# Performance work log

Hardware: AMD Instinct MI355X
Metric: run time of the kernel (lower is better)

## Reference

```python
import jax, jax.numpy as jnp
import numpy as np
from jax import lax
import math

B, C, H, W = 8, 512, 24, 24
L = H * W
D_STATE = 16
D_INNER = 2 * C
DT_RANK = C // 16
K = 4
SCALE = 1.0 / math.sqrt(C)


def layer_norm(x, g, b, eps=1e-5):
    m = x.mean(-1, keepdims=True)
    v = ((x - m) ** 2).mean(-1, keepdims=True)
    return (x - m) * lax.rsqrt(v + eps) * g + b


def selective_scan(u, delta, A, Bm, Cm, Ds):
    # u, delta: (B,K,d,L); Bm, Cm: (B,K,N,L); A: (K,d,N); Ds: (K,d)
    us = jnp.moveaxis(u, -1, 0)      # (L,B,K,d)
    dts = jnp.moveaxis(delta, -1, 0)
    Bs = jnp.moveaxis(Bm, -1, 0)     # (L,B,K,N)
    Cs = jnp.moveaxis(Cm, -1, 0)

    def step(h, inp):
        u_t, dt_t, B_t, C_t = inp
        dA = jnp.exp(dt_t[..., None] * A)                      # (B,K,d,N)
        dBu = (dt_t * u_t)[..., None] * B_t[:, :, None, :]     # (B,K,d,N)
        h = dA * h + dBu
        y = jnp.einsum('bkdn,bkn->bkd', h, C_t)
        return h, y

    h0 = jnp.zeros(u.shape[:3] + (A.shape[-1],), u.dtype)
    _, ys = lax.scan(step, h0, (us, dts, Bs, Cs))
    y = jnp.moveaxis(ys, 0, -1)                                # (B,K,d,L)
    return y + Ds[None, :, :, None] * u


def ss2d(x, in_proj_w, dwconv_w, dwconv_b, x_proj_w, dt_proj_w, dt_proj_b,
         A_logs, Ds, out_norm_g, out_norm_b, out_proj_w):
    # x: (B,H,W,C) channel-last
    xz = x @ in_proj_w.T                                       # (B,H,W,2*d_inner)
    xi, z = jnp.split(xz, 2, axis=-1)
    xc = xi.transpose(0, 3, 1, 2)                              # (B,d_inner,H,W)
    xc = lax.conv_general_dilated(xc, dwconv_w, (1, 1), 'SAME',
                                  feature_group_count=D_INNER,
                                  dimension_numbers=('NCHW', 'OIHW', 'NCHW'))
    xc = jax.nn.silu(xc + dwconv_b[None, :, None, None])
    x_hw = xc.reshape(B, D_INNER, L)
    x_wh = xc.transpose(0, 1, 3, 2).reshape(B, D_INNER, L)
    xs = jnp.stack([x_hw, x_wh, x_hw[..., ::-1], x_wh[..., ::-1]], axis=1)  # (B,4,d,L)
    x_dbl = jnp.einsum('bkdl,kcd->bkcl', xs, x_proj_w)
    dt, Bm, Cm = jnp.split(x_dbl, [DT_RANK, DT_RANK + D_STATE], axis=2)
    delta = jax.nn.softplus(jnp.einsum('bkrl,kdr->bkdl', dt, dt_proj_w)
                            + dt_proj_b[None, :, :, None])
    A = -jnp.exp(A_logs)
    ys = selective_scan(xs, delta, A, Bm, Cm, Ds)              # (B,4,d,L)
    y_wh = ys[:, 1].reshape(B, D_INNER, W, H).transpose(0, 1, 3, 2).reshape(B, D_INNER, L)
    y_whr = ys[:, 3, :, ::-1].reshape(B, D_INNER, W, H).transpose(0, 1, 3, 2).reshape(B, D_INNER, L)
    y = ys[:, 0] + ys[:, 2, :, ::-1] + y_wh + y_whr
    y = y.reshape(B, D_INNER, H, W).transpose(0, 2, 3, 1)      # (B,H,W,d_inner)
    y = layer_norm(y, out_norm_g, out_norm_b)
    y = y * jax.nn.silu(z)
    return y @ out_proj_w.T                                    # (B,H,W,C)


def setup_inputs():
    key = jax.random.key(0)
    ks = jax.random.split(key, 10)
    n = lambda k, sh, s=0.02: jax.random.normal(k, sh, dtype=jnp.float32) * s
    return {
        'x5': jax.random.normal(ks[0], (B, C, H, W), dtype=jnp.float32),
        'conv_w': n(ks[1], (C, C)),
        'conv_b': jnp.zeros((C,), jnp.float32),
        'ln1_g': jnp.ones((C,), jnp.float32),
        'ln1_b': jnp.zeros((C,), jnp.float32),
        'in_proj_w': n(ks[2], (2 * D_INNER, C)),
        'dwconv_w': n(ks[3], (D_INNER, 1, 3, 3), 0.1),
        'dwconv_b': jnp.zeros((D_INNER,), jnp.float32),
        'x_proj_w': n(ks[4], (K, DT_RANK + 2 * D_STATE, D_INNER)),
        'dt_proj_w': n(ks[5], (K, D_INNER, DT_RANK), 0.1),
        'dt_proj_b': n(ks[6], (K, D_INNER), 0.1),
        'A_logs': jnp.tile(jnp.log(jnp.arange(1, D_STATE + 1, dtype=jnp.float32))[None, None, :],
                           (K, D_INNER, 1)),
        'Ds': jnp.ones((K, D_INNER), jnp.float32),
        'out_norm_g': jnp.ones((D_INNER,), jnp.float32),
        'out_norm_b': jnp.zeros((D_INNER,), jnp.float32),
        'out_proj_w': n(ks[7], (C, D_INNER)),
    }


def reference(x5, conv_w, conv_b, ln1_g, ln1_b, in_proj_w, dwconv_w, dwconv_b,
              x_proj_w, dt_proj_w, dt_proj_b, A_logs, Ds, out_norm_g, out_norm_b,
              out_proj_w):
    # 1x1 conv + residual
    x5 = jnp.einsum('bchw,oc->bohw', x5, conv_w) + conv_b[None, :, None, None] + x5
    x0 = x5.transpose(0, 2, 3, 1)                              # (B,H,W,C)
    # VSSBlock: x + SS2D(LN(x)); called twice on same input with same weights -> identical
    x00 = x0 + ss2d(layer_norm(x0, ln1_g, ln1_b), in_proj_w, dwconv_w, dwconv_b,
                    x_proj_w, dt_proj_w, dt_proj_b, A_logs, Ds,
                    out_norm_g, out_norm_b, out_proj_w)
    xq = x00.transpose(0, 3, 1, 2).reshape(B, C, L)            # (B,C,L)
    xq_flat = xq.transpose(0, 2, 1).reshape(B * L, C)          # (B*L, C)
    xk_flat = xq.transpose(1, 0, 2).reshape(C, B * L)          # (C, B*L)
    xw = (xq_flat @ xk_flat) * SCALE                           # (B*L, B*L)
    xw = xw.reshape(B * L, B, L).max(-1).mean(-1).reshape(B, L)
    xw = jax.nn.softmax(xw, axis=-1)
    norm0 = x5 / jnp.maximum(jnp.linalg.norm(x5, axis=1, keepdims=True), 1e-12)
    xw = xw[:, None, :]                                        # (B,1,L)
    xw_max = xw.max(-1, keepdims=True)
    mask = (xw == xw_max).astype(x5.dtype).reshape(B, 1, H, W)  # winner-take-all
    seeds = (norm0 * mask).sum((2, 3))                         # (B,C)
    # correlation (eval branch: relu), seeds act as 1x1 conv weights
    cor = jax.nn.relu(jnp.einsum('bchw,oc->bohw', norm0, seeds)).mean(1).reshape(B, L)
    mn = cor.min(1, keepdims=True)
    mx = cor.max(1, keepdims=True)
    cormap = ((cor - mn) / (mx - mn + 1e-12)).reshape(B, 1, H, W)
    x51 = x5 * cormap
    proto1 = x51.mean((0, 2, 3), keepdims=True)                # (1,C,1,1)
    return (x5, proto1, x5 * proto1 + x51, mask)
```

## Files before the change

### kernel.cpp

```cpp
#include <hip/hip_runtime.h>
#include <math.h>

#define NB 8
#define NC 512
#define NH 24
#define NW 24
#define NL 576
#define ND 1024
#define NBL 4608
#define NCH 8
#define CL 72

static constexpr float SCALE_ = 0.044194173824159216f;

typedef __attribute__((ext_vector_type(8))) short bf16x8;
typedef __attribute__((ext_vector_type(4))) float f32x4;

__device__ __forceinline__ unsigned enc_f(float f){
    unsigned u = __float_as_uint(f);
    return (u & 0x80000000u) ? ~u : (u | 0x80000000u);
}
__device__ __forceinline__ float dec_f(unsigned e){
    return (e & 0x80000000u) ? __uint_as_float(e ^ 0x80000000u) : __uint_as_float(~e);
}

__device__ __forceinline__ int scan_idx(int t, int k){
    int t2 = (k >= 2) ? (NL - 1 - t) : t;
    return (k & 1) ? ((t2 % NH) * NW + t2 / NH) : t2;
}

__device__ __forceinline__ float softplus_f(float x){
    return fmaxf(x, 0.f) + __logf(1.f + __expf(-fabsf(x)));
}
__device__ __forceinline__ float silu_f(float x){
    return x / (1.f + __expf(-x));
}

__device__ __forceinline__ void split_bf(float v, unsigned short &h, unsigned short &l){
    unsigned u = __float_as_uint(v);
    unsigned hr = (u + 0x7fffu + ((u>>16)&1u)) >> 16;
    h = (unsigned short)hr;
    float hf = __uint_as_float(hr << 16);
    unsigned u2 = __float_as_uint(v - hf);
    l = (unsigned short)((u2 + 0x7fffu + ((u2>>16)&1u)) >> 16);
}

__global__ void k_transpose_in(const float* __restrict__ x5, float* __restrict__ x5t,
                               unsigned short* __restrict__ x5tB){
    __shared__ float t[32][33];
    const int b = blockIdx.z;
    const int c0 = blockIdx.x*32, l0 = blockIdx.y*32;
    const int tx = threadIdx.x & 31, ty = threadIdx.x >> 5;
    #pragma unroll
    for (int i=ty; i<32; i+=8)
        t[i][tx] = x5[((size_t)b*NC + c0 + i)*NL + l0 + tx];
    __syncthreads();
    #pragma unroll
    for (int i=ty; i<32; i+=8){
        float v = t[tx][i];
        x5t[((size_t)b*NL + l0 + i)*NC + c0 + tx] = v;
        unsigned short hh, ll; split_bf(v, hh, ll);
        size_t rb = ((size_t)b*NL + l0 + i)*1536 + c0 + tx;
        x5tB[rb] = hh; x5tB[rb+512] = ll; x5tB[rb+1024] = hh;
    }
}

template<int FORM>
__global__ void k_split(const float* __restrict__ in, unsigned short* __restrict__ oA,
                        unsigned short* __restrict__ oB, int K, int total4){
    int t = blockIdx.x*256 + threadIdx.x;
    if (t >= total4) return;
    int kq = K >> 2;
    int r = t / kq; int k4 = (t - r*kq) << 2;
    float4 v = *(const float4*)(in + (size_t)r*K + k4);
    float vv[4] = {v.x, v.y, v.z, v.w};
    unsigned short h[4], lo[4];
    #pragma unroll
    for (int i=0;i<4;i++) split_bf(vv[i], h[i], lo[i]);
    unsigned hp0 = h[0] | ((unsigned)h[1]<<16), hp1 = h[2] | ((unsigned)h[3]<<16);
    unsigned lp0 = lo[0] | ((unsigned)lo[1]<<16), lp1 = lo[2] | ((unsigned)lo[3]<<16);
    size_t base = (size_t)r*3*K + k4;
    if (FORM == 0 || FORM == 2){
        unsigned* p0 = (unsigned*)(oA + base);
        unsigned* p1 = (unsigned*)(oA + base + K);
        unsigned* p2 = (unsigned*)(oA + base + 2*K);
        p0[0]=hp0; p0[1]=hp1;  p1[0]=hp0; p1[1]=hp1;  p2[0]=lp0; p2[1]=lp1;
    }
    if (FORM == 1 || FORM == 2){
        unsigned short* o = (FORM==2) ? oB : oA;
        unsigned* p0 = (unsigned*)(o + base);
        unsigned* p1 = (unsigned*)(o + base + K);
        unsigned* p2 = (unsigned*)(o + base + 2*K);
        p0[0]=hp0; p0[1]=hp1;  p1[0]=lp0; p1[1]=lp1;  p2[0]=hp0; p2[1]=hp1;
    }
}

template<int MODE>
__launch_bounds__(256)
__global__ void mfma_nt(const unsigned short* __restrict__ A, const unsigned short* __restrict__ Bm,
                        const float* __restrict__ R0, const float* __restrict__ R1,
                        float* __restrict__ out0, float* __restrict__ out1,
                        unsigned* __restrict__ mbuf, int K3)
{
    int bi, bj;
    if (MODE == 4){
        int rem = blockIdx.x, len = 36; bi = 0;
        while (rem >= len){ rem -= len; len--; bi++; }
        bj = bi + rem;
    } else { bi = blockIdx.x; bj = blockIdx.y; }
    const int m0 = bi*128, n0 = bj*128;
    __shared__ __align__(16) unsigned short As[128*32];
    __shared__ __align__(16) unsigned short Bs[128*32];
    const int tid = threadIdx.x;
    const int w = tid >> 6, l = tid & 63;
    const int mw = (w>>1)*64, nw = (w&1)*64;
    const int fr = l & 15, fq = l >> 4;

    f32x4 acc[4][4];
    #pragma unroll
    for (int i=0;i<4;i++)
        #pragma unroll
        for (int j=0;j<4;j++)
            #pragma unroll
            for (int c=0;c<4;c++) acc[i][j][c] = 0.f;

    const int c0 = tid, c1 = tid + 256;
    const int r0 = c0 >> 2, o0 = (c0 & 3) * 8;
    const int r1 = c1 >> 2, o1 = (c1 & 3) * 8;
    const unsigned short* pA0 = A  + (size_t)(m0 + r0)*K3 + o0;
    const unsigned short* pA1 = A  + (size_t)(m0 + r1)*K3 + o1;
    const unsigned short* pB0 = Bm + (size_t)(n0 + r0)*K3 + o0;
    const unsigned short* pB1 = Bm + (size_t)(n0 + r1)*K3 + o1;

    float4 a0 = *(const float4*)(pA0);
    float4 a1 = *(const float4*)(pA1);
    float4 b0 = *(const float4*)(pB0);
    float4 b1 = *(const float4*)(pB1);

    for (int k0 = 0; k0 < K3; k0 += 32){
        __syncthreads();
        *(float4*)&As[c0*8] = a0;
        *(float4*)&As[c1*8] = a1;
        *(float4*)&Bs[c0*8] = b0;
        *(float4*)&Bs[c1*8] = b1;
        __syncthreads();
        if (k0 + 32 < K3){
            a0 = *(const float4*)(pA0 + k0 + 32);
            a1 = *(const float4*)(pA1 + k0 + 32);
            b0 = *(const float4*)(pB0 + k0 + 32);
            b1 = *(const float4*)(pB1 + k0 + 32);
        }
        bf16x8 af[4], bf[4];
        #pragma unroll
        for (int i=0;i<4;i++){
            af[i] = *(const bf16x8*)&As[(mw + i*16 + fr)*32 + fq*8];
            bf[i] = *(const bf16x8*)&Bs[(nw + i*16 + fr)*32 + fq*8];
        }
        #pragma unroll
        for (int i=0;i<4;i++)
            #pragma unroll
            for (int j=0;j<4;j++)
                acc[i][j] = __builtin_amdgcn_mfma_f32_16x16x32_bf16(af[i], bf[j], acc[i][j], 0, 0, 0);
    }

    if (MODE == 4){
        const int b2c = (n0 + nw) / NL;
        #pragma unroll
        for (int mi=0; mi<4; mi++){
            #pragma unroll
            for (int i=0;i<4;i++){
                float v = fmaxf(fmaxf(acc[mi][0][i], acc[mi][1][i]),
                                fmaxf(acc[mi][2][i], acc[mi][3][i]));
                v = fmaxf(v, __shfl_xor(v, 1));
                v = fmaxf(v, __shfl_xor(v, 2));
                v = fmaxf(v, __shfl_xor(v, 4));
                v = fmaxf(v, __shfl_xor(v, 8));
                if (fr == 0)
                    atomicMax(&mbuf[(size_t)(m0 + mw + mi*16 + fq*4 + i)*NB + b2c], enc_f(v));
            }
        }
        const int b2r = (m0 + mw) / NL;
        #pragma unroll
        for (int ni=0; ni<4; ni++){
            float cm = -3.4e38f;
            #pragma unroll
            for (int mi=0; mi<4; mi++)
                #pragma unroll
                for (int i=0;i<4;i++) cm = fmaxf(cm, acc[mi][ni][i]);
            cm = fmaxf(cm, __shfl_xor(cm, 16));
            cm = fmaxf(cm, __shfl_xor(cm, 32));
            if (fq == 0)
                atomicMax(&mbuf[(size_t)(n0 + nw + ni*16 + fr)*NB + b2r], enc_f(cm));
        }
        return;
    }

    #pragma unroll
    for (int mi=0; mi<4; mi++){
        const int m = m0 + mw + mi*16 + fq*4;
        #pragma unroll
        for (int ni=0; ni<4; ni++){
            const int n = n0 + nw + ni*16 + fr;
            f32x4 a = acc[mi][ni];
            if (MODE == 0){
                float4 cb = *(const float4*)(R0 + m);
                float4 rs = *(const float4*)(R1 + (size_t)n*NC + m);
                float4 ov = make_float4(a[0]+cb.x+rs.x, a[1]+cb.y+rs.y, a[2]+cb.z+rs.z, a[3]+cb.w+rs.w);
                *(float4*)(out0 + (size_t)n*NC + m) = ov;
            } else if (MODE == 1){
                float4 ov = make_float4(a[0], a[1], a[2], a[3]);
                if (m < ND) *(float4*)(out0 + (size_t)n*ND + m) = ov;
                else        *(float4*)(out1 + (size_t)n*ND + (m - ND)) = ov;
            } else {
                float4 rs = *(const float4*)(R1 + (size_t)n*NC + m);
                float4 ov = make_float4(a[0]+rs.x, a[1]+rs.y, a[2]+rs.z, a[3]+rs.w);
                *(float4*)(out0 + (size_t)n*NC + m) = ov;
            }
        }
    }
}

template<int MODE>
__launch_bounds__(256)
__global__ void gemm_nt(const float* __restrict__ A0, const float* __restrict__ B0,
                        const float* __restrict__ R,
                        float* __restrict__ out0, float* __restrict__ out1,
                        unsigned* __restrict__ mbuf, int K)
{
    __shared__ __align__(16) float As[16][68];
    __shared__ __align__(16) float Bs[16][68];
    const int tid = threadIdx.x;
    const int m0 = blockIdx.x * 64;
    const int n0 = blockIdx.y * 64;
    const float* A = A0;
    const float* B = B0;
    int kdir = 0;
    if (MODE == 2) {
        const int bk = blockIdx.z;
        kdir = bk & 3; const int bb = bk >> 2;
        A = A0 + (size_t)kdir * 64 * 1024;
        B = B0 + (size_t)bb * NL * 1024;
    }
    const int lrow = tid >> 2;
    const int lk4  = (tid & 3) << 2;
    int brow = n0 + lrow;
    if (MODE == 2) brow = scan_idx(brow, kdir);
    const float* aptr = A + (size_t)(m0 + lrow) * K + lk4;
    const float* bptr = B + (size_t)brow * K + lk4;

    float acc[4][4];
    #pragma unroll
    for (int i=0;i<4;i++){
        #pragma unroll
        for (int j=0;j<4;j++) acc[i][j]=0.f;
    }
    const int tx = tid & 15, ty = tid >> 4;

    for (int k0 = 0; k0 < K; k0 += 16) {
        float4 av = *(const float4*)(aptr + k0);
        float4 bv = *(const float4*)(bptr + k0);
        __syncthreads();
        As[lk4+0][lrow]=av.x; As[lk4+1][lrow]=av.y; As[lk4+2][lrow]=av.z; As[lk4+3][lrow]=av.w;
        Bs[lk4+0][lrow]=bv.x; Bs[lk4+1][lrow]=bv.y; Bs[lk4+2][lrow]=bv.z; Bs[lk4+3][lrow]=bv.w;
        __syncthreads();
        #pragma unroll
        for (int kk=0;kk<16;kk++){
            float4 a = *(const float4*)&As[kk][ty<<2];
            float4 b = *(const float4*)&Bs[kk][tx<<2];
            acc[0][0] = fmaf(a.x,b.x,acc[0][0]); acc[0][1] = fmaf(a.x,b.y,acc[0][1]);
            acc[0][2] = fmaf(a.x,b.z,acc[0][2]); acc[0][3] = fmaf(a.x,b.w,acc[0][3]);
            acc[1][0] = fmaf(a.y,b.x,acc[1][0]); acc[1][1] = fmaf(a.y,b.y,acc[1][1]);
            acc[1][2] = fmaf(a.y,b.z,acc[1][2]); acc[1][3] = fmaf(a.y,b.w,acc[1][3]);
            acc[2][0] = fmaf(a.z,b.x,acc[2][0]); acc[2][1] = fmaf(a.z,b.y,acc[2][1]);
            acc[2][2] = fmaf(a.z,b.z,acc[2][2]); acc[2][3] = fmaf(a.z,b.w,acc[2][3]);
            acc[3][0] = fmaf(a.w,b.x,acc[3][0]); acc[3][1] = fmaf(a.w,b.y,acc[3][1]);
            acc[3][2] = fmaf(a.w,b.z,acc[3][2]); acc[3][3] = fmaf(a.w,b.w,acc[3][3]);
        }
    }

    #pragma unroll
    for (int j=0;j<4;j++){
        const int n  = n0 + (tx<<2) + j;
        const int mm = m0 + (ty<<2);
        float4 v = make_float4(acc[0][j], acc[1][j], acc[2][j], acc[3][j]);
        if (MODE == 2){
            *(float4*)(out0 + ((size_t)blockIdx.z*NL + n)*64 + mm) = v;
        }
    }
}

__global__ void k_ln512b(const float* __restrict__ x, const float* __restrict__ g,
                         const float* __restrict__ bb, unsigned short* __restrict__ outB){
    int n = blockIdx.x; int tid = threadIdx.x;
    const float* row = x + (size_t)n*NC;
    float v0 = row[tid], v1 = row[tid+256];
    __shared__ float s1[256], s2[256];
    s1[tid] = v0+v1; s2[tid] = v0*v0 + v1*v1;
    __syncthreads();
    for (int s=128;s>0;s>>=1){ if (tid<s){ s1[tid]+=s1[tid+s]; s2[tid]+=s2[tid+s]; } __syncthreads(); }
    float mean = s1[0]*(1.f/NC);
    float var  = fmaxf(s2[0]*(1.f/NC) - mean*mean, 0.f);
    float rs   = rsqrtf(var + 1e-5f);
    float r0 = (v0-mean)*rs*g[tid]     + bb[tid];
    float r1 = (v1-mean)*rs*g[tid+256] + bb[tid+256];
    unsigned short h0,l0,h1,l1; split_bf(r0,h0,l0); split_bf(r1,h1,l1);
    size_t base = (size_t)n*1536;
    outB[base+tid]     =h0; outB[base+512+tid]     =l0; outB[base+1024+tid]     =h0;
    outB[base+tid+256] =h1; outB[base+512+tid+256] =l1; outB[base+1024+tid+256] =h1;
}

__global__ void k_dwconv(const float* __restrict__ xi, const float* __restrict__ w,
                         const float* __restrict__ bias, float* __restrict__ xcl){
    int d = blockIdx.x*256 + threadIdx.x;
    int h = blockIdx.y; int b = blockIdx.z;
    float W[9];
    #pragma unroll
    for (int i=0;i<9;i++) W[i] = w[d*9+i];
    float bs = bias[d];
    const size_t rb = ((size_t)b*NL)*ND + d;
    const bool hm = h > 0, hp = h < NH-1;
    float p0=0.f,p1=0.f,p2=0.f;
    float c0 = hm ? xi[rb + (size_t)((h-1)*NW)*ND] : 0.f;
    float c1 = xi[rb + (size_t)(h*NW)*ND];
    float c2 = hp ? xi[rb + (size_t)((h+1)*NW)*ND] : 0.f;
    for (int wc=0; wc<NW; wc++){
        float n0,n1,n2;
        if (wc < NW-1){
            n0 = hm ? xi[rb + (size_t)((h-1)*NW+wc+1)*ND] : 0.f;
            n1 = xi[rb + (size_t)(h*NW+wc+1)*ND];
            n2 = hp ? xi[rb + (size_t)((h+1)*NW+wc+1)*ND] : 0.f;
        } else { n0=0.f;n1=0.f;n2=0.f; }
        float acc = bs;
        acc = fmaf(W[0],p0, fmaf(W[1],c0, fmaf(W[2],n0, acc)));
        acc = fmaf(W[3],p1, fmaf(W[4],c1, fmaf(W[5],n1, acc)));
        acc = fmaf(W[6],p2, fmaf(W[7],c2, fmaf(W[8],n2, acc)));
        xcl[rb + (size_t)(h*NW+wc)*ND] = silu_f(acc);
        p0=c0;p1=c1;p2=c2; c0=n0;c1=n1;c2=n2;
    }
}

#define DA_POWERS \
    float e2=e1*e1; float e3=e2*e1; float e4=e2*e2; \
    float e6=e4*e2; float e7=e4*e3; float e8=e4*e4; float e12=e8*e4; \
    float dA[16]; \
    dA[0]=e1; dA[1]=e2; dA[2]=e3; dA[3]=e4; dA[4]=e4*e1; dA[5]=e6; dA[6]=e7; dA[7]=e8; \
    dA[8]=e8*e1; dA[9]=e8*e2; dA[10]=e8*e3; dA[11]=e12; dA[12]=e12*e1; dA[13]=e12*e2; \
    dA[14]=e12*e3; dA[15]=e8*e8;

#define DOT4(rq, dtb, out) { \
    float4 q0=rq[0],q1=rq[1],q2=rq[2],q3=rq[3],q4=rq[4],q5=rq[5],q6=rq[6],q7=rq[7]; \
    float s0=0.f,s1=0.f,s2=0.f,s3=0.f; \
    s0=fmaf(q0.x,wdt[0],s0);  s1=fmaf(q0.y,wdt[1],s1);  s2=fmaf(q0.z,wdt[2],s2);  s3=fmaf(q0.w,wdt[3],s3); \
    s0=fmaf(q1.x,wdt[4],s0);  s1=fmaf(q1.y,wdt[5],s1);  s2=fmaf(q1.z,wdt[6],s2);  s3=fmaf(q1.w,wdt[7],s3); \
    s0=fmaf(q2.x,wdt[8],s0);  s1=fmaf(q2.y,wdt[9],s1);  s2=fmaf(q2.z,wdt[10],s2); s3=fmaf(q2.w,wdt[11],s3); \
    s0=fmaf(q3.x,wdt[12],s0); s1=fmaf(q3.y,wdt[13],s1); s2=fmaf(q3.z,wdt[14],s2); s3=fmaf(q3.w,wdt[15],s3); \
    s0=fmaf(q4.x,wdt[16],s0); s1=fmaf(q4.y,wdt[17],s1); s2=fmaf(q4.z,wdt[18],s2); s3=fmaf(q4.w,wdt[19],s3); \
    s0=fmaf(q5.x,wdt[20],s0); s1=fmaf(q5.y,wdt[21],s1); s2=fmaf(q5.z,wdt[22],s2); s3=fmaf(q5.w,wdt[23],s3); \
    s0=fmaf(q6.x,wdt[24],s0); s1=fmaf(q6.y,wdt[25],s1); s2=fmaf(q6.z,wdt[26],s2); s3=fmaf(q6.w,wdt[27],s3); \
    s0=fmaf(q7.x,wdt[28],s0); s1=fmaf(q7.y,wdt[29],s1); s2=fmaf(q7.z,wdt[30],s2); s3=fmaf(q7.w,wdt[31],s3); \
    out = (s0+s1)+(s2+s3)+dtb; }

__launch_bounds__(128)
__global__ void k_scan_p1(const float* __restrict__ xcl, const float* __restrict__ xdbl,
                          const float* __restrict__ dtw, const float* __restrict__ dtb,
                          const float* __restrict__ alogs,
                          float* __restrict__ hfin, float* __restrict__ prodA){
    const int d = blockIdx.x*128 + threadIdx.x;
    const int chunk = blockIdx.y;
    const int bk = blockIdx.z;
    const int k = bk & 3, b = bk >> 2;
    const int kd = k*ND + d;
    float wdt[32];
    {
        const float4* p = (const float4*)(dtw + (size_t)kd*32);
        #pragma unroll
        for (int i=0;i<8;i++){ float4 v=p[i]; wdt[4*i]=v.x; wdt[4*i+1]=v.y; wdt[4*i+2]=v.z; wdt[4*i+3]=v.w; }
    }
    float An[16]; bool ladder = true;
    {
        const float4* p = (const float4*)(alogs + (size_t)kd*16);
        #pragma unroll
        for (int i=0;i<4;i++){
            float4 v=p[i];
            An[4*i]=-__expf(v.x); An[4*i+1]=-__expf(v.y); An[4*i+2]=-__expf(v.z); An[4*i+3]=-__expf(v.w);
        }
        #pragma unroll
        for (int n=0;n<16;n++) ladder = ladder && (fabsf(An[n] + (float)(n+1)) < 1e-3f*(n+1));
    }
    const float dtbias = dtb[kd];
    __shared__ __align__(16) float rows[CL*64];
    {
        const float4* src = (const float4*)(xdbl + ((size_t)bk*NL + chunk*CL)*64);
        for (int i = threadIdx.x; i < CL*16; i += 128) ((float4*)rows)[i] = src[i];
    }
    __syncthreads();
    float h[16], pA[16];
    #pragma unroll
    for (int n=0;n<16;n++){ h[n]=0.f; pA[n]=1.f; }
    if (ladder){
        float u = xcl[((size_t)b*NL + scan_idx(chunk*CL, k))*ND + d];
        for (int t=0;t<CL;t++){
            const float4* rq = (const float4*)(rows + t*64);
            float dr; DOT4(rq, dtbias, dr);
            float u_cur = u;
            if (t+1 < CL) u = xcl[((size_t)b*NL + scan_idx(chunk*CL+t+1, k))*ND + d];
            float sp = softplus_f(dr);
            float du = sp * u_cur;
            float e1 = __expf(-sp);
            DA_POWERS
            float4 B0=rq[8],B1=rq[9],B2=rq[10],B3=rq[11];
            const float Bv[16] = {B0.x,B0.y,B0.z,B0.w,B1.x,B1.y,B1.z,B1.w,
                                  B2.x,B2.y,B2.z,B2.w,B3.x,B3.y,B3.z,B3.w};
            #pragma unroll
            for (int n=0;n<16;n++){
                pA[n] *= dA[n];
                h[n] = fmaf(dA[n], h[n], du*Bv[n]);
            }
        }
    } else {
        for (int t=0;t<CL;t++){
            const float4* rq = (const float4*)(rows + t*64);
            float dr; DOT4(rq, dtbias, dr);
            float sp = softplus_f(dr);
            int idx = scan_idx(chunk*CL + t, k);
            float u  = xcl[((size_t)b*NL + idx)*ND + d];
            float du = sp * u;
            const float* row = rows + t*64;
            #pragma unroll
            for (int n=0;n<16;n++){
                float dA = __expf(sp * An[n]);
                pA[n] *= dA;
                h[n] = fmaf(dA, h[n], du*row[32+n]);
            }
        }
    }
    size_t base = (size_t)(bk*NCH + chunk)*16*1024 + d;
    #pragma unroll
    for (int n=0;n<16;n++){ hfin[base + n*1024] = h[n]; prodA[base + n*1024] = pA[n]; }
}

__global__ void k_scan_mid(float* __restrict__ hfin, const float* __restrict__ prodA){
    int id = blockIdx.x*256 + threadIdx.x;
    int d = id & 1023, nn = (id >> 10) & 15, bk = id >> 14;
    float h = 0.f;
    for (int j=0;j<NCH;j++){
        size_t idx = (size_t)((bk*NCH + j)*16 + nn)*1024 + d;
        float hf = hfin[idx], pa = prodA[idx];
        hfin[idx] = h;
        h = fmaf(pa, h, hf);
    }
}

__launch_bounds__(128)
__global__ void k_scan_p2(const float* __restrict__ xcl, const float* __restrict__ xdbl,
                          const float* __restrict__ dtw, const float* __restrict__ dtb,
                          const float* __restrict__ alogs,
                          const float* __restrict__ hfin, float* __restrict__ yacc){
    const int d = blockIdx.x*128 + threadIdx.x;
    const int chunk = blockIdx.y;
    const int bk = blockIdx.z;
    const int k = bk & 3, b = bk >> 2;
    const int kd = k*ND + d;
    float wdt[32];
    {
        const float4* p = (const float4*)(dtw + (size_t)kd*32);
        #pragma unroll
        for (int i=0;i<8;i++){ float4 v=p[i]; wdt[4*i]=v.x; wdt[4*i+1]=v.y; wdt[4*i+2]=v.z; wdt[4*i+3]=v.w; }
    }
    float An[16]; bool ladder = true;
    {
        const float4* p = (const float4*)(alogs + (size_t)kd*16);
        #pragma unroll
        for (int i=0;i<4;i++){
            float4 v=p[i];
            An[4*i]=-__expf(v.x); An[4*i+1]=-__expf(v.y); An[4*i+2]=-__expf(v.z); An[4*i+3]=-__expf(v.w);
        }
        #pragma unroll
        for (int n=0;n<16;n++) ladder = ladder && (fabsf(An[n] + (float)(n+1)) < 1e-3f*(n+1));
    }
    const float dtbias = dtb[kd];
    __shared__ __align__(16) float rows[CL*64];
    {
        const float4* src = (const float4*)(xdbl + ((size_t)bk*NL + chunk*CL)*64);
        for (int i = threadIdx.x; i < CL*16; i += 128) ((float4*)rows)[i] = src[i];
    }
    __syncthreads();
    float h[16];
    {
        size_t base = (size_t)(bk*NCH + chunk)*16*1024 + d;
        #pragma unroll
        for (int n=0;n<16;n++) h[n] = hfin[base + n*1024];
    }
    if (ladder){
        int idx = scan_idx(chunk*CL, k);
        float u = xcl[((size_t)b*NL + idx)*ND + d];
        for (int t=0;t<CL;t++){
            const float4* rq = (const float4*)(rows + t*64);
            float dr; DOT4(rq, dtbias, dr);
            float u_cur = u; int idx_cur = idx;
            if (t+1 < CL){
                idx = scan_idx(chunk*CL+t+1, k);
                u = xcl[((size_t)b*NL + idx)*ND + d];
            }
            float sp = softplus_f(dr);
            float du = sp * u_cur;
            float e1 = __expf(-sp);
            DA_POWERS
            float4 B0=rq[8],B1=rq[9],B2=rq[10],B3=rq[11];
            float4 C0=rq[12],C1=rq[13],C2=rq[14],C3=rq[15];
            const float Bv[16] = {B0.x,B0.y,B0.z,B0.w,B1.x,B1.y,B1.z,B1.w,
                                  B2.x,B2.y,B2.z,B2.w,B3.x,B3.y,B3.z,B3.w};
            const float Cv[16] = {C0.x,C0.y,C0.z,C0.w,C1.x,C1.y,C1.z,C1.w,
                                  C2.x,C2.y,C2.z,C2.w,C3.x,C3.y,C3.z,C3.w};
            float y0=0.f, y1=0.f;
            #pragma unroll
            for (int n=0;n<16;n++){
                h[n] = fmaf(dA[n], h[n], du*Bv[n]);
                if (n & 1) y1 = fmaf(h[n], Cv[n], y1); else y0 = fmaf(h[n], Cv[n], y0);
            }
            atomicAdd(&yacc[((size_t)b*NL + idx_cur)*ND + d], y0+y1);
        }
    } else {
        for (int t=0;t<CL;t++){
            const float4* rq = (const float4*)(rows + t*64);
            float dr; DOT4(rq, dtbias, dr);
            float sp = softplus_f(dr);
            int idx = scan_idx(chunk*CL + t, k);
            size_t base = ((size_t)b*NL + idx)*ND + d;
            float u  = xcl[base];
            float du = sp * u;
            const float* row = rows + t*64;
            float y = 0.f;
            #pragma unroll
            for (int n=0;n<16;n++){
                float dA = __expf(sp * An[n]);
                h[n] = fmaf(dA, h[n], du*row[32+n]);
                y = fmaf(h[n], row[48+n], y);
            }
            atomicAdd(&yacc[base], y);
        }
    }
}

__global__ void k_combine(const float* __restrict__ y, const float* __restrict__ xcl,
                          const float* __restrict__ Ds,
                          const float* __restrict__ g, const float* __restrict__ bb,
                          const float* __restrict__ z, unsigned short* __restrict__ zB){
    int n = blockIdx.x;
    size_t base = (size_t)n*ND;
    int tid = threadIdx.x;
    float v[4]; float sum=0.f, sq=0.f;
    #pragma unroll
    for (int j=0;j<4;j++){
        int d = tid + 256*j;
        float ds = Ds[d] + Ds[ND+d] + Ds[2*ND+d] + Ds[3*ND+d];
        float val = y[base+d] + ds*xcl[base+d];
        v[j]=val; sum+=val; sq+=val*val;
    }
    __shared__ float s1[256], s2[256];
    s1[tid]=sum; s2[tid]=sq; __syncthreads();
    for (int st=128;st>0;st>>=1){ if(tid<st){ s1[tid]+=s1[tid+st]; s2[tid]+=s2[tid+st]; } __syncthreads(); }
    float mean = s1[0]*(1.f/ND);
    float var  = fmaxf(s2[0]*(1.f/ND) - mean*mean, 0.f);
    float rs   = rsqrtf(var + 1e-5f);
    size_t zb = (size_t)n*3072;
    #pragma unroll
    for (int j=0;j<4;j++){
        int d = tid + 256*j;
        float ln = (v[j]-mean)*rs*g[d] + bb[d];
        float res = ln * silu_f(z[base+d]);
        unsigned short hh,ll; split_bf(res,hh,ll);
        zB[zb + d] = hh; zB[zb + 1024 + d] = ll; zB[zb + 2048 + d] = hh;
    }
}

__global__ void k_xwpre(const unsigned* __restrict__ M, float* __restrict__ xwp){
    int n = blockIdx.x*256 + threadIdx.x; if (n >= NBL) return;
    float sum = 0.f;
    #pragma unroll
    for (int b2=0;b2<NB;b2++) sum += dec_f(M[(size_t)n*NB + b2]);
    xwp[n] = sum * (SCALE_/8.f);
}

__global__ void k_mask(const float* __restrict__ xwp, float* __restrict__ maskf){
    int b = blockIdx.x; int tid = threadIdx.x;
    float m = -1e30f;
    for (int i=tid;i<NL;i+=64) m = fmaxf(m, xwp[b*NL+i]);
    __shared__ float s1[64];
    s1[tid]=m; __syncthreads();
    for (int st=32;st>0;st>>=1){ if(tid<st) s1[tid]=fmaxf(s1[tid],s1[tid+st]); __syncthreads(); }
    float bm = s1[0];
    for (int i=tid;i<NL;i+=64) maskf[b*NL+i] = (xwp[b*NL+i]==bm) ? 1.f : 0.f;
}

__global__ void k_norm0(const float* __restrict__ x5r, float* __restrict__ norm0){
    int n = blockIdx.x; int tid = threadIdx.x;
    float v0 = x5r[(size_t)n*NC+tid], v1 = x5r[(size_t)n*NC+tid+256];
    __shared__ float s1[256];
    s1[tid] = v0*v0 + v1*v1; __syncthreads();
    for (int st=128;st>0;st>>=1){ if(tid<st) s1[tid]+=s1[tid+st]; __syncthreads(); }
    float inv = 1.f / fmaxf(sqrtf(s1[0]), 1e-12f);
    norm0[(size_t)n*NC+tid]     = v0*inv;
    norm0[(size_t)n*NC+tid+256] = v1*inv;
}

__global__ void k_seeds(const float* __restrict__ norm0, const float* __restrict__ maskf,
                        float* __restrict__ seeds){
    int b = blockIdx.x; int c = threadIdx.x;
    float acc = 0.f;
    for (int l=0;l<NL;l++){
        float mk = maskf[b*NL+l];
        if (mk != 0.f) acc += norm0[((size_t)b*NL+l)*NC + c]*mk;
    }
    seeds[b*NC + c] = acc;
}

__global__ void k_cor(const float* __restrict__ norm0, const float* __restrict__ seeds,
                      float* __restrict__ cor){
    int n = blockIdx.x; int tid = threadIdx.x;
    int o = tid >> 6, lane = tid & 63;
    float acc = 0.f;
    #pragma unroll
    for (int i=0;i<8;i++){
        int c = lane + 64*i;
        acc += norm0[(size_t)n*NC + c] * seeds[o*NC + c];
    }
    #pragma unroll
    for (int s=32;s>0;s>>=1) acc += __shfl_xor(acc, s);
    __shared__ float sr[8];
    if (lane == 0) sr[o] = fmaxf(acc, 0.f);
    __syncthreads();
    if (tid == 0){
        float r = 0.f;
        #pragma unroll
        for (int o2=0;o2<8;o2++) r += sr[o2];
        cor[n] = r * (1.f/8.f);
    }
}

__global__ void k_cormap(const float* __restrict__ cor, float* __restrict__ cmap){
    int b = blockIdx.x, tid = threadIdx.x;
    float mn = 1e30f, mx = -1e30f;
    for (int i=tid;i<NL;i+=64){ float v=cor[b*NL+i]; mn=fminf(mn,v); mx=fmaxf(mx,v); }
    __shared__ float sn[64], sx[64];
    sn[tid]=mn; sx[tid]=mx; __syncthreads();
    for (int st=32;st>0;st>>=1){ if(tid<st){ sn[tid]=fminf(sn[tid],sn[tid+st]); sx[tid]=fmaxf(sx[tid],sx[tid+st]); } __syncthreads(); }
    float MN=sn[0], MX=sx[0];
    float inv = 1.f/(MX-MN+1e-12f);
    for (int i=tid;i<NL;i+=64) cmap[b*NL+i] = (cor[b*NL+i]-MN)*inv;
}

__global__ void k_proto(const float* __restrict__ x5r, const float* __restrict__ cmap,
                        float* __restrict__ pacc){
    int c = threadIdx.x;
    int chunk = blockIdx.x;
    float acc = 0.f;
    for (int i=0;i<64;i++){
        int n = chunk*64 + i;
        acc += x5r[(size_t)n*NC + c] * cmap[n];
    }
    atomicAdd(&pacc[c], acc);
}

__global__ void k_final(const float* __restrict__ x5r, const float* __restrict__ cmap,
                        const float* __restrict__ pacc, const float* __restrict__ maskf,
                        float* __restrict__ out){
    int id = blockIdx.x*256 + threadIdx.x;
    int l = id % NL; int bc = id / NL; int c = bc & 511; int b = bc >> 9;
    float v  = x5r[((size_t)b*NL + l)*NC + c];
    float p  = pacc[c] * (1.f/(float)NBL);
    float cm = cmap[b*NL + l];
    out[id] = v;
    out[2359296 + 512 + id] = v*(p + cm);
    if (id < 512)  out[2359296 + id] = pacc[id] * (1.f/(float)NBL);
    if (id < NBL)  out[2359296 + 512 + 2359296 + id] = maskf[id];
}

extern "C" void kernel_launch(void* const* d_in, const int* in_sizes, int n_in,
                              void* d_out, int out_size, void* d_ws, size_t ws_size,
                              hipStream_t stream) {
    const float* x5        = (const float*)d_in[0];
    const float* conv_w    = (const float*)d_in[1];
    const float* conv_b    = (const float*)d_in[2];
    const float* ln1_g     = (const float*)d_in[3];
    const float* ln1_b     = (const float*)d_in[4];
    const float* in_proj_w = (const float*)d_in[5];
    const float* dwconv_w  = (const float*)d_in[6];
    const float* dwconv_b  = (const float*)d_in[7];
    const float* x_proj_w  = (const float*)d_in[8];
    const float* dt_proj_w = (const float*)d_in[9];
    const float* dt_proj_b = (const float*)d_in[10];
    const float* A_logs    = (const float*)d_in[11];
    const float* Ds        = (const float*)d_in[12];
    const float* out_norm_g= (const float*)d_in[13];
    const float* out_norm_b= (const float*)d_in[14];
    const float* out_proj_w= (const float*)d_in[15];

    float* ws = (float*)d_ws;
    const size_t O_X5R  = 0;
    const size_t O_XLN  = 2359296;
    const size_t O_XI   = 4718592;
    const size_t O_Z    = 9437184;
    const size_t O_XCL  = 14155776;
    const size_t O_XDBL = 18874368;
    const size_t O_HF   = 20054016;
    const size_t O_PA   = 24248320;
    const size_t O_MBUF = 28442624;
    const size_t O_XWP  = 28479488;
    const size_t O_MASK = 28484096;
    const size_t O_COR  = 28488704;
    const size_t O_CMAP = 28493312;
    const size_t O_SEED = 28497920;
    const size_t O_PACC = 28502016;

    float* x5r  = ws + O_X5R;
    float* xqf  = ws + O_XLN;
    float* xi   = ws + O_XI;
    float* yacc = ws + O_XI;
    unsigned short* wAo = (unsigned short*)(ws + O_XI);
    float* z    = ws + O_Z;
    float* xcl  = ws + O_XCL;
    unsigned short* wAi = (unsigned short*)(ws + O_XCL);
    float* nrm0 = ws + O_XCL;
    float* xdbl = ws + O_XDBL;
    float* x5t  = ws + O_HF;
    float* hfin = ws + O_HF;
    unsigned short* xlnB = (unsigned short*)(ws + O_HF);
    unsigned short* zB   = (unsigned short*)(ws + O_HF);
    unsigned short* xqfA = (unsigned short*)(ws + O_HF);
    float* prodA = ws + O_PA;
    unsigned short* x5tB = (unsigned short*)(ws + O_PA);
    unsigned short* wAc  = (unsigned short*)(ws + O_PA) + 7077888;
    unsigned short* xqfB = (unsigned short*)(ws + O_PA);
    unsigned* mbuf = (unsigned*)(ws + O_MBUF);
    float* xwp  = ws + O_XWP;
    float* maskf= ws + O_MASK;
    float* cor  = ws + O_COR;
    float* cmap = ws + O_CMAP;
    float* seeds= ws + O_SEED;
    float* pacc = ws + O_PACC;

    (void)hipMemsetAsync(mbuf, 0, 36864*sizeof(unsigned), stream);
    (void)hipMemsetAsync(pacc, 0, 512*sizeof(float), stream);

    k_transpose_in<<<dim3(16,18,8), 256, 0, stream>>>(x5, x5t, x5tB);
    k_split<0><<<256, 256, 0, stream>>>(conv_w, wAc, nullptr, 512, 65536);
    mfma_nt<0><<<dim3(4,36), 256, 0, stream>>>(wAc, x5tB, conv_b, x5t, x5r, nullptr, nullptr, 1536);
    k_ln512b<<<NBL, 256, 0, stream>>>(x5r, ln1_g, ln1_b, xlnB);
    k_split<0><<<1024, 256, 0, stream>>>(in_proj_w, wAi, nullptr, 512, 262144);
    mfma_nt<1><<<dim3(16,36), 256, 0, stream>>>(wAi, xlnB, nullptr, nullptr, xi, z, nullptr, 1536);
    k_dwconv<<<dim3(4,NH,NB), 256, 0, stream>>>(xi, dwconv_w, dwconv_b, xcl);
    (void)hipMemsetAsync(yacc, 0, (size_t)4718592*sizeof(float), stream);
    gemm_nt<2><<<dim3(1,9,32), 256, 0, stream>>>(x_proj_w, xcl, nullptr, xdbl, nullptr, nullptr, 1024);
    k_scan_p1<<<dim3(8,NCH,32), 128, 0, stream>>>(xcl, xdbl, dt_proj_w, dt_proj_b, A_logs, hfin, prodA);
    k_scan_mid<<<2048, 256, 0, stream>>>(hfin, prodA);
    k_scan_p2<<<dim3(8,NCH,32), 128, 0, stream>>>(xcl, xdbl, dt_proj_w, dt_proj_b, A_logs, hfin, yacc);
    k_combine<<<NBL, 256, 0, stream>>>(yacc, xcl, Ds, out_norm_g, out_norm_b, z, zB);
    k_split<0><<<512, 256, 0, stream>>>(out_proj_w, wAo, nullptr, 1024, 131072);
    mfma_nt<3><<<dim3(4,36), 256, 0, stream>>>(wAo, zB, nullptr, x5r, xqf, nullptr, nullptr, 3072);
    k_split<2><<<2304, 256, 0, stream>>>(xqf, xqfA, xqfB, 512, 589824);
    mfma_nt<4><<<666, 256, 0, stream>>>(xqfA, xqfB, nullptr, nullptr, nullptr, nullptr, mbuf, 1536);
    k_xwpre<<<18, 256, 0, stream>>>(mbuf, xwp);
    k_mask<<<NB, 64, 0, stream>>>(xwp, maskf);
    k_norm0<<<NBL, 256, 0, stream>>>(x5r, nrm0);
    k_seeds<<<NB, 512, 0, stream>>>(nrm0, maskf, seeds);
    k_cor<<<NBL, 512, 0, stream>>>(nrm0, seeds, cor);
    k_cormap<<<NB, 64, 0, stream>>>(cor, cmap);
    k_proto<<<72, 512, 0, stream>>>(x5r, cmap, pacc);
    k_final<<<9216, 256, 0, stream>>>(x5r, cmap, pacc, maskf, (float*)d_out);
}
```

Baseline: 652.0 us.

## Pack scan math into float2 vectors, fuse xw reduction into mask, sparse seeds

The scan kernels' ladder path now uses two-wide float vectors for the dt dot product, the dA powers, the state update and the output reduction, aiming to emit packed FP32 instructions on MI355X. The separate xw pre-reduction and mask kernels are merged into one kernel that also records the winning indices, saving one launch and one intermediate buffer. The seeds kernel then loops only over the recorded hits instead of all 576 positions. Floating-point summation order changes slightly, and hit order depends on shared atomics.

```diff
diff --git a/kernel.cpp b/kernel.cpp
--- a/kernel.cpp
+++ b/kernel.cpp
@@ -11,10 +11,9 @@
 #define NCH 8
 #define CL 72
 
-static constexpr float SCALE_ = 0.044194173824159216f;
-
 typedef __attribute__((ext_vector_type(8))) short bf16x8;
 typedef __attribute__((ext_vector_type(4))) float f32x4;
+typedef __attribute__((ext_vector_type(2))) float f32x2;
 
 __device__ __forceinline__ unsigned enc_f(float f){
     unsigned u = __float_as_uint(f);
@@ -339,26 +338,22 @@
     }
 }
 
-#define DA_POWERS \
+#define DA_POWERS2 \
     float e2=e1*e1; float e3=e2*e1; float e4=e2*e2; \
     float e6=e4*e2; float e7=e4*e3; float e8=e4*e4; float e12=e8*e4; \
-    float dA[16]; \
-    dA[0]=e1; dA[1]=e2; dA[2]=e3; dA[3]=e4; dA[4]=e4*e1; dA[5]=e6; dA[6]=e7; dA[7]=e8; \
-    dA[8]=e8*e1; dA[9]=e8*e2; dA[10]=e8*e3; dA[11]=e12; dA[12]=e12*e1; dA[13]=e12*e2; \
-    dA[14]=e12*e3; dA[15]=e8*e8;
-
-#define DOT4(rq, dtb, out) { \
-    float4 q0=rq[0],q1=rq[1],q2=rq[2],q3=rq[3],q4=rq[4],q5=rq[5],q6=rq[6],q7=rq[7]; \
-    float s0=0.f,s1=0.f,s2=0.f,s3=0.f; \
-    s0=fmaf(q0.x,wdt[0],s0);  s1=fmaf(q0.y,wdt[1],s1);  s2=fmaf(q0.z,wdt[2],s2);  s3=fmaf(q0.w,wdt[3],s3); \
-    s0=fmaf(q1.x,wdt[4],s0);  s1=fmaf(q1.y,wdt[5],s1);  s2=fmaf(q1.z,wdt[6],s2);  s3=fmaf(q1.w,wdt[7],s3); \
-    s0=fmaf(q2.x,wdt[8],s0);  s1=fmaf(q2.y,wdt[9],s1);  s2=fmaf(q2.z,wdt[10],s2); s3=fmaf(q2.w,wdt[11],s3); \
-    s0=fmaf(q3.x,wdt[12],s0); s1=fmaf(q3.y,wdt[13],s1); s2=fmaf(q3.z,wdt[14],s2); s3=fmaf(q3.w,wdt[15],s3); \
-    s0=fmaf(q4.x,wdt[16],s0); s1=fmaf(q4.y,wdt[17],s1); s2=fmaf(q4.z,wdt[18],s2); s3=fmaf(q4.w,wdt[19],s3); \
-    s0=fmaf(q5.x,wdt[20],s0); s1=fmaf(q5.y,wdt[21],s1); s2=fmaf(q5.z,wdt[22],s2); s3=fmaf(q5.w,wdt[23],s3); \
-    s0=fmaf(q6.x,wdt[24],s0); s1=fmaf(q6.y,wdt[25],s1); s2=fmaf(q6.z,wdt[26],s2); s3=fmaf(q6.w,wdt[27],s3); \
-    s0=fmaf(q7.x,wdt[28],s0); s1=fmaf(q7.y,wdt[29],s1); s2=fmaf(q7.z,wdt[30],s2); s3=fmaf(q7.w,wdt[31],s3); \
-    out = (s0+s1)+(s2+s3)+dtb; }
+    f32x2 dA2[8]; \
+    dA2[0]=(f32x2){e1,e2};       dA2[1]=(f32x2){e3,e4}; \
+    dA2[2]=(f32x2){e4*e1,e6};    dA2[3]=(f32x2){e7,e8}; \
+    dA2[4]=(f32x2){e8*e1,e8*e2}; dA2[5]=(f32x2){e8*e3,e12}; \
+    dA2[6]=(f32x2){e12*e1,e12*e2}; dA2[7]=(f32x2){e12*e3,e8*e8};
+
+#define DOT4P(rq2, dtb, out) { \
+    f32x2 sA={0.f,0.f},sB={0.f,0.f},sC={0.f,0.f},sD={0.f,0.f}; \
+    sA += rq2[0]*wdt2[0];  sB += rq2[1]*wdt2[1];  sC += rq2[2]*wdt2[2];  sD += rq2[3]*wdt2[3]; \
+    sA += rq2[4]*wdt2[4];  sB += rq2[5]*wdt2[5];  sC += rq2[6]*wdt2[6];  sD += rq2[7]*wdt2[7]; \
+    sA += rq2[8]*wdt2[8];  sB += rq2[9]*wdt2[9];  sC += rq2[10]*wdt2[10]; sD += rq2[11]*wdt2[11]; \
+    sA += rq2[12]*wdt2[12]; sB += rq2[13]*wdt2[13]; sC += rq2[14]*wdt2[14]; sD += rq2[15]*wdt2[15]; \
+    out = ((sA.x+sA.y)+(sB.x+sB.y)) + ((sC.x+sC.y)+(sD.x+sD.y)) + dtb; }
 
 __launch_bounds__(128)
 __global__ void k_scan_p1(const float* __restrict__ xcl, const float* __restrict__ xdbl,
@@ -370,11 +365,15 @@
     const int bk = blockIdx.z;
     const int k = bk & 3, b = bk >> 2;
     const int kd = k*ND + d;
-    float wdt[32];
+    f32x2 wdt2[16];
     {
         const float4* p = (const float4*)(dtw + (size_t)kd*32);
         #pragma unroll
-        for (int i=0;i<8;i++){ float4 v=p[i]; wdt[4*i]=v.x; wdt[4*i+1]=v.y; wdt[4*i+2]=v.z; wdt[4*i+3]=v.w; }
+        for (int i=0;i<8;i++){
+            float4 v=p[i];
+            wdt2[2*i]   = (f32x2){v.x, v.y};
+            wdt2[2*i+1] = (f32x2){v.z, v.w};
+        }
     }
     float An[16]; bool ladder = true;
     {
@@ -394,33 +393,40 @@
         for (int i = threadIdx.x; i < CL*16; i += 128) ((float4*)rows)[i] = src[i];
     }
     __syncthreads();
-    float h[16], pA[16];
-    #pragma unroll
-    for (int n=0;n<16;n++){ h[n]=0.f; pA[n]=1.f; }
     if (ladder){
+        f32x2 h2[8], pA2[8];
+        #pragma unroll
+        for (int n=0;n<8;n++){ h2[n]=(f32x2){0.f,0.f}; pA2[n]=(f32x2){1.f,1.f}; }
         float u = xcl[((size_t)b*NL + scan_idx(chunk*CL, k))*ND + d];
         for (int t=0;t<CL;t++){
-            const float4* rq = (const float4*)(rows + t*64);
-            float dr; DOT4(rq, dtbias, dr);
+            const f32x2* rq2 = (const f32x2*)(rows + t*64);
+            float dr; DOT4P(rq2, dtbias, dr);
             float u_cur = u;
             if (t+1 < CL) u = xcl[((size_t)b*NL + scan_idx(chunk*CL+t+1, k))*ND + d];
             float sp = softplus_f(dr);
             float du = sp * u_cur;
             float e1 = __expf(-sp);
-            DA_POWERS
-            float4 B0=rq[8],B1=rq[9],B2=rq[10],B3=rq[11];
-            const float Bv[16] = {B0.x,B0.y,B0.z,B0.w,B1.x,B1.y,B1.z,B1.w,
-                                  B2.x,B2.y,B2.z,B2.w,B3.x,B3.y,B3.z,B3.w};
-            #pragma unroll
-            for (int n=0;n<16;n++){
-                pA[n] *= dA[n];
-                h[n] = fmaf(dA[n], h[n], du*Bv[n]);
+            DA_POWERS2
+            f32x2 du2 = (f32x2){du, du};
+            #pragma unroll
+            for (int n=0;n<8;n++){
+                pA2[n] *= dA2[n];
+                h2[n] = dA2[n]*h2[n] + du2*rq2[16+n];
             }
         }
+        size_t base = (size_t)(bk*NCH + chunk)*16*1024 + d;
+        #pragma unroll
+        for (int n=0;n<8;n++){
+            hfin[base + (2*n)*1024]   = h2[n].x;  hfin[base + (2*n+1)*1024] = h2[n].y;
+            prodA[base + (2*n)*1024]  = pA2[n].x; prodA[base + (2*n+1)*1024]= pA2[n].y;
+        }
     } else {
+        float h[16], pA[16];
+        #pragma unroll
+        for (int n=0;n<16;n++){ h[n]=0.f; pA[n]=1.f; }
         for (int t=0;t<CL;t++){
-            const float4* rq = (const float4*)(rows + t*64);
-            float dr; DOT4(rq, dtbias, dr);
+            const f32x2* rq2 = (const f32x2*)(rows + t*64);
+            float dr; DOT4P(rq2, dtbias, dr);
             float sp = softplus_f(dr);
             int idx = scan_idx(chunk*CL + t, k);
             float u  = xcl[((size_t)b*NL + idx)*ND + d];
@@ -433,10 +439,10 @@
                 h[n] = fmaf(dA, h[n], du*row[32+n]);
             }
         }
-    }
-    size_t base = (size_t)(bk*NCH + chunk)*16*1024 + d;
-    #pragma unroll
-    for (int n=0;n<16;n++){ hfin[base + n*1024] = h[n]; prodA[base + n*1024] = pA[n]; }
+        size_t base = (size_t)(bk*NCH + chunk)*16*1024 + d;
+        #pragma unroll
+        for (int n=0;n<16;n++){ hfin[base + n*1024] = h[n]; prodA[base + n*1024] = pA[n]; }
+    }
 }
 
 __global__ void k_scan_mid(float* __restrict__ hfin, const float* __restrict__ prodA){
@@ -461,11 +467,15 @@
     const int bk = blockIdx.z;
     const int k = bk & 3, b = bk >> 2;
     const int kd = k*ND + d;
-    float wdt[32];
+    f32x2 wdt2[16];
     {
         const float4* p = (const float4*)(dtw + (size_t)kd*32);
         #pragma unroll
-        for (int i=0;i<8;i++){ float4 v=p[i]; wdt[4*i]=v.x; wdt[4*i+1]=v.y; wdt[4*i+2]=v.z; wdt[4*i+3]=v.w; }
+        for (int i=0;i<8;i++){
+            float4 v=p[i];
+            wdt2[2*i]   = (f32x2){v.x, v.y};
+            wdt2[2*i+1] = (f32x2){v.z, v.w};
+        }
     }
     float An[16]; bool ladder = true;
     {
@@ -485,18 +495,19 @@
         for (int i = threadIdx.x; i < CL*16; i += 128) ((float4*)rows)[i] = src[i];
     }
     __syncthreads();
-    float h[16];
-    {
-        size_t base = (size_t)(bk*NCH + chunk)*16*1024 + d;
-        #pragma unroll
-        for (int n=0;n<16;n++) h[n] = hfin[base + n*1024];
-    }
     if (ladder){
+        f32x2 h2[8];
+        {
+            size_t base = (size_t)(bk*NCH + chunk)*16*1024 + d;
+            #pragma unroll
+            for (int n=0;n<8;n++)
+                h2[n] = (f32x2){hfin[base + (2*n)*1024], hfin[base + (2*n+1)*1024]};
+        }
         int idx = scan_idx(chunk*CL, k);
         float u = xcl[((size_t)b*NL + idx)*ND + d];
         for (int t=0;t<CL;t++){
-            const float4* rq = (const float4*)(rows + t*64);
-            float dr; DOT4(rq, dtbias, dr);
+            const f32x2* rq2 = (const f32x2*)(rows + t*64);
+            float dr; DOT4P(rq2, dtbias, dr);
             float u_cur = u; int idx_cur = idx;
             if (t+1 < CL){
                 idx = scan_idx(chunk*CL+t+1, k);
@@ -505,25 +516,26 @@
             float sp = softplus_f(dr);
             float du = sp * u_cur;
             float e1 = __expf(-sp);
-            DA_POWERS
-            float4 B0=rq[8],B1=rq[9],B2=rq[10],B3=rq[11];
-            float4 C0=rq[12],C1=rq[13],C2=rq[14],C3=rq[15];
-            const float Bv[16] = {B0.x,B0.y,B0.z,B0.w,B1.x,B1.y,B1.z,B1.w,
-                                  B2.x,B2.y,B2.z,B2.w,B3.x,B3.y,B3.z,B3.w};
-            const float Cv[16] = {C0.x,C0.y,C0.z,C0.w,C1.x,C1.y,C1.z,C1.w,
-                                  C2.x,C2.y,C2.z,C2.w,C3.x,C3.y,C3.z,C3.w};
-            float y0=0.f, y1=0.f;
-            #pragma unroll
-            for (int n=0;n<16;n++){
-                h[n] = fmaf(dA[n], h[n], du*Bv[n]);
-                if (n & 1) y1 = fmaf(h[n], Cv[n], y1); else y0 = fmaf(h[n], Cv[n], y0);
+            DA_POWERS2
+            f32x2 du2 = (f32x2){du, du};
+            f32x2 y2 = (f32x2){0.f, 0.f};
+            #pragma unroll
+            for (int n=0;n<8;n++){
+                h2[n] = dA2[n]*h2[n] + du2*rq2[16+n];
+                y2 += h2[n]*rq2[24+n];
             }
-            atomicAdd(&yacc[((size_t)b*NL + idx_cur)*ND + d], y0+y1);
+            atomicAdd(&yacc[((size_t)b*NL + idx_cur)*ND + d], y2.x + y2.y);
         }
     } else {
+        float h[16];
+        {
+            size_t base = (size_t)(bk*NCH + chunk)*16*1024 + d;
+            #pragma unroll
+            for (int n=0;n<16;n++) h[n] = hfin[base + n*1024];
+        }
         for (int t=0;t<CL;t++){
-            const float4* rq = (const float4*)(rows + t*64);
-            float dr; DOT4(rq, dtbias, dr);
+            const f32x2* rq2 = (const f32x2*)(rows + t*64);
+            float dr; DOT4P(rq2, dtbias, dr);
             float sp = softplus_f(dr);
             int idx = scan_idx(chunk*CL + t, k);
             size_t base = ((size_t)b*NL + idx)*ND + d;
@@ -574,23 +586,36 @@
     }
 }
 
-__global__ void k_xwpre(const unsigned* __restrict__ M, float* __restrict__ xwp){
-    int n = blockIdx.x*256 + threadIdx.x; if (n >= NBL) return;
-    float sum = 0.f;
-    #pragma unroll
-    for (int b2=0;b2<NB;b2++) sum += dec_f(M[(size_t)n*NB + b2]);
-    xwp[n] = sum * (SCALE_/8.f);
-}
-
-__global__ void k_mask(const float* __restrict__ xwp, float* __restrict__ maskf){
+__global__ void k_mask2(const unsigned* __restrict__ M, float* __restrict__ maskf,
+                        int* __restrict__ hitcnt, int* __restrict__ hitidx){
     int b = blockIdx.x; int tid = threadIdx.x;
-    float m = -1e30f;
-    for (int i=tid;i<NL;i+=64) m = fmaxf(m, xwp[b*NL+i]);
-    __shared__ float s1[64];
-    s1[tid]=m; __syncthreads();
-    for (int st=32;st>0;st>>=1){ if(tid<st) s1[tid]=fmaxf(s1[tid],s1[tid+st]); __syncthreads(); }
-    float bm = s1[0];
-    for (int i=tid;i<NL;i+=64) maskf[b*NL+i] = (xwp[b*NL+i]==bm) ? 1.f : 0.f;
+    __shared__ int lcnt;
+    if (tid == 0) lcnt = 0;
+    __syncthreads();
+    float loc[9];
+    float m = -3.4e38f;
+    #pragma unroll
+    for (int j=0;j<9;j++){
+        int l = tid + j*64;
+        float s = 0.f;
+        #pragma unroll
+        for (int b2=0;b2<NB;b2++) s += dec_f(M[(size_t)(b*NL+l)*NB + b2]);
+        loc[j] = s; m = fmaxf(m, s);
+    }
+    #pragma unroll
+    for (int s=32;s>0;s>>=1) m = fmaxf(m, __shfl_xor(m, s));
+    #pragma unroll
+    for (int j=0;j<9;j++){
+        int l = tid + j*64;
+        bool hit = (loc[j] == m);
+        maskf[b*NL + l] = hit ? 1.f : 0.f;
+        if (hit){
+            int pos = atomicAdd(&lcnt, 1);
+            hitidx[b*NL + pos] = l;
+        }
+    }
+    __syncthreads();
+    if (tid == 0) hitcnt[b] = lcnt;
 }
 
 __global__ void k_norm0(const float* __restrict__ x5r, float* __restrict__ norm0){
@@ -604,13 +629,14 @@
     norm0[(size_t)n*NC+tid+256] = v1*inv;
 }
 
-__global__ void k_seeds(const float* __restrict__ norm0, const float* __restrict__ maskf,
-                        float* __restrict__ seeds){
+__global__ void k_seeds(const float* __restrict__ norm0, const int* __restrict__ hitcnt,
+                        const int* __restrict__ hitidx, float* __restrict__ seeds){
     int b = blockIdx.x; int c = threadIdx.x;
+    int cnt = hitcnt[b];
     float acc = 0.f;
-    for (int l=0;l<NL;l++){
-        float mk = maskf[b*NL+l];
-        if (mk != 0.f) acc += norm0[((size_t)b*NL+l)*NC + c]*mk;
+    for (int i=0;i<cnt;i++){
+        int l = hitidx[b*NL + i];
+        acc += norm0[((size_t)b*NL+l)*NC + c];
     }
     seeds[b*NC + c] = acc;
 }
@@ -706,12 +732,13 @@
     const size_t O_HF   = 20054016;
     const size_t O_PA   = 24248320;
     const size_t O_MBUF = 28442624;
-    const size_t O_XWP  = 28479488;
     const size_t O_MASK = 28484096;
     const size_t O_COR  = 28488704;
     const size_t O_CMAP = 28493312;
     const size_t O_SEED = 28497920;
     const size_t O_PACC = 28502016;
+    const size_t O_HITC = 28502528;
+    const size_t O_HITI = 28502544;
 
     float* x5r  = ws + O_X5R;
     float* xqf  = ws + O_XLN;
@@ -733,12 +760,13 @@
     unsigned short* wAc  = (unsigned short*)(ws + O_PA) + 7077888;
     unsigned short* xqfB = (unsigned short*)(ws + O_PA);
     unsigned* mbuf = (unsigned*)(ws + O_MBUF);
-    float* xwp  = ws + O_XWP;
     float* maskf= ws + O_MASK;
     float* cor  = ws + O_COR;
     float* cmap = ws + O_CMAP;
     float* seeds= ws + O_SEED;
     float* pacc = ws + O_PACC;
+    int* hitcnt = (int*)(ws + O_HITC);
+    int* hitidx = (int*)(ws + O_HITI);
 
     (void)hipMemsetAsync(mbuf, 0, 36864*sizeof(unsigned), stream);
     (void)hipMemsetAsync(pacc, 0, 512*sizeof(float), stream);
@@ -760,10 +788,9 @@
     mfma_nt<3><<<dim3(4,36), 256, 0, stream>>>(wAo, zB, nullptr, x5r, xqf, nullptr, nullptr, 3072);
     k_split<2><<<2304, 256, 0, stream>>>(xqf, xqfA, xqfB, 512, 589824);
     mfma_nt<4><<<666, 256, 0, stream>>>(xqfA, xqfB, nullptr, nullptr, nullptr, nullptr, mbuf, 1536);
-    k_xwpre<<<18, 256, 0, stream>>>(mbuf, xwp);
-    k_mask<<<NB, 64, 0, stream>>>(xwp, maskf);
+    k_mask2<<<NB, 64, 0, stream>>>(mbuf, maskf, hitcnt, hitidx);
     k_norm0<<<NBL, 256, 0, stream>>>(x5r, nrm0);
-    k_seeds<<<NB, 512, 0, stream>>>(nrm0, maskf, seeds);
+    k_seeds<<<NB, 512, 0, stream>>>(nrm0, hitcnt, hitidx, seeds);
     k_cor<<<NBL, 512, 0, stream>>>(nrm0, seeds, cor);
     k_cormap<<<NB, 64, 0, stream>>>(cor, cmap);
     k_proto<<<72, 512, 0, stream>>>(x5r, cmap, pacc);
```

After: 616.8 us. 1.06x faster.
